# Performance work log

Hardware: AMD Instinct MI355X
Metric: run time of the kernel (lower is better)

The kernel has to match this reference:

```python
import jax, jax.numpy as jnp
import numpy as np

SEQ_LEN = 2048
DIM = 1024
DIM_HEAD = 64
NHEAD = DIM // DIM_HEAD


def setup_inputs() -> dict:
    key = jax.random.key(0)
    k1, k2, k3 = jax.random.split(key, 3)
    x = jax.random.normal(k1, (SEQ_LEN, DIM), dtype=jnp.float32)
    # ortho_init approximated by scaled gaussian weights (same math path in forward)
    Wqkv = jax.random.normal(k2, (DIM, 3 * DIM), dtype=jnp.float32) / np.sqrt(DIM)
    Wout = jax.random.normal(k3, (DIM, DIM), dtype=jnp.float32) / np.sqrt(DIM)
    bias = jnp.zeros((DIM,), dtype=jnp.float32)
    return {"x": x, "Wqkv": Wqkv, "Wout": Wout, "bias": bias}


def reference(x, Wqkv, Wout, bias):
    seq_len = x.shape[-2]
    qkv = x @ Wqkv  # [S, 3*dim]
    qkv = jnp.reshape(qkv, (-1, 3, NHEAD, DIM_HEAD))  # [S,3,H,D]
    qkv = jnp.swapaxes(qkv, 0, 2)  # [H,3,S,D]
    q, k, v = (jax.lax.index_in_dim(qkv, i, -3, keepdims=False) for i in range(3))
    # [H,S,S] full logits, scaled
    logits = q @ jnp.swapaxes(k, -1, -2) / jnp.sqrt(DIM_HEAD)
    mask = jnp.tril(jnp.ones((seq_len, seq_len), dtype=jnp.float32))
    logits = jnp.where(mask, logits, jnp.finfo(logits.dtype).min)
    dtype = logits.dtype
    probs = jax.nn.softmax(logits.astype(jnp.float32), axis=-1).astype(dtype)
    attn_outs = probs @ v  # [H,S,D]
    attn_outs = jnp.reshape(jnp.swapaxes(attn_outs, 0, 1), (-1, NHEAD * DIM_HEAD))
    return attn_outs @ Wout + bias
```

## Files before the change

kernel.cpp:

```cpp
#include <hip/hip_runtime.h>
#include <cstdint>

#define SEQ_LEN 2048
#define DIM 1024
#define NHEAD 16
#define DHEAD 64
#define QKV_LD (3 * DIM)

typedef unsigned short u16;
typedef short bf16x8 __attribute__((ext_vector_type(8)));
typedef float f32x4 __attribute__((ext_vector_type(4)));

__device__ __forceinline__ u16 f2bf(float f) {
    union { float f; unsigned u; } v;
    v.f = f;
    unsigned r = v.u + 0x7fff + ((v.u >> 16) & 1);
    return (u16)(r >> 16);
}

__device__ __forceinline__ void load_lds16(const void* g, void* l) {
    __builtin_amdgcn_global_load_lds(
        (const __attribute__((address_space(1))) void*)g,
        (__attribute__((address_space(3))) void*)l, 16, 0, 0);
}

__global__ __launch_bounds__(256) void cast_bf16_k(const float* __restrict__ in,
                                                   u16* __restrict__ out, int n4) {
    const int i = blockIdx.x * 256 + threadIdx.x;
    if (i < n4) {
        const float4 v = reinterpret_cast<const float4*>(in)[i];
        const unsigned p0 = (unsigned)f2bf(v.x) | ((unsigned)f2bf(v.y) << 16);
        const unsigned p1 = (unsigned)f2bf(v.z) | ((unsigned)f2bf(v.w) << 16);
        reinterpret_cast<uint2*>(out)[i] = make_uint2(p0, p1);
    }
}

__global__ __launch_bounds__(256) void transpose_cast_k(const float* __restrict__ W,
                                                        u16* __restrict__ Wt,
                                                        int K, int N) {
    __shared__ float tile[32][33];
    const int n0 = blockIdx.x * 32, k0 = blockIdx.y * 32;
    const int tx = threadIdx.x & 31, ty = threadIdx.x >> 5;
#pragma unroll
    for (int i = 0; i < 32; i += 8)
        tile[ty + i][tx] = W[(k0 + ty + i) * N + n0 + tx];
    __syncthreads();
#pragma unroll
    for (int i = 0; i < 32; i += 8)
        Wt[(n0 + ty + i) * K + k0 + tx] = f2bf(tile[tx][ty + i]);
}

template <int MODE, int BM, int BN>
__global__ __launch_bounds__(256) void gemm_bf16(const u16* __restrict__ A,
                                                 const u16* __restrict__ Bt,
                                                 const float* __restrict__ bias,
                                                 void* __restrict__ Cout,
                                                 int M, int N, int K) {
    constexpr int AI = BM / 32;
    constexpr int BJ = BN / 32;
    constexpr int ASZ = BM * 64;
    constexpr int BSZ = BN * 64;
    __shared__ u16 As[2 * ASZ];
    __shared__ u16 Bs[2 * BSZ];

    const int t = threadIdx.x;
    const int lane = t & 63;
    const int quad = lane >> 4;
    const int l15 = lane & 15;
    const int w = t >> 6;
    const int wm = (w & 1) * (BM / 2);
    const int wn = (w >> 1) * (BN / 2);
    const int m0 = blockIdx.y * BM;
    const int n0 = blockIdx.x * BN;
    const int sr = t >> 2;
    const int sc = (t & 3) << 3;

    const u16* Ab = A + (size_t)(m0 + sr) * K + sc;
    const u16* Bb = Bt + (size_t)(n0 + sr) * K + sc;

    auto stage = [&](int buf, int k0) {
#pragma unroll
        for (int kc = 0; kc < 2; ++kc) {
#pragma unroll
            for (int c = 0; c < BM / 64; ++c)
                load_lds16(Ab + (size_t)(c * 64) * K + k0 + kc * 32,
                           &As[buf * ASZ + kc * BM * 32 + c * 2048 + t * 8]);
#pragma unroll
            for (int c = 0; c < BN / 64; ++c)
                load_lds16(Bb + (size_t)(c * 64) * K + k0 + kc * 32,
                           &Bs[buf * BSZ + kc * BN * 32 + c * 2048 + t * 8]);
        }
    };

    stage(0, 0);
    f32x4 acc[AI][BJ] = {};

    const int niter = K / 64;
    for (int it = 0; it < niter; ++it) {
        const int cur = it & 1, nxt = cur ^ 1;
        __syncthreads();
        if (it + 1 < niter) stage(nxt, (it + 1) * 64);
#pragma unroll
        for (int kc = 0; kc < 2; ++kc) {
            bf16x8 af[AI], bfr[BJ];
#pragma unroll
            for (int i = 0; i < AI; ++i)
                af[i] = *reinterpret_cast<const bf16x8*>(
                    &As[cur * ASZ + kc * BM * 32 + (wm + i * 16 + l15) * 32 + quad * 8]);
#pragma unroll
            for (int j = 0; j < BJ; ++j)
                bfr[j] = *reinterpret_cast<const bf16x8*>(
                    &Bs[cur * BSZ + kc * BN * 32 + (wn + j * 16 + l15) * 32 + quad * 8]);
#pragma unroll
            for (int i = 0; i < AI; ++i)
#pragma unroll
                for (int j = 0; j < BJ; ++j)
                    acc[i][j] =
                        __builtin_amdgcn_mfma_f32_16x16x32_bf16(af[i], bfr[j], acc[i][j], 0, 0, 0);
        }
    }

#pragma unroll
    for (int j = 0; j < BJ; ++j) {
        const int col = n0 + wn + j * 16 + l15;
        float bv = 0.f;
        if constexpr (MODE == 1) bv = bias[col];
#pragma unroll
        for (int i = 0; i < AI; ++i) {
            const int row = m0 + wm + i * 16 + quad * 4;
#pragma unroll
            for (int r = 0; r < 4; ++r) {
                const float v = acc[i][j][r];
                if constexpr (MODE == 1)
                    ((float*)Cout)[(size_t)(row + r) * N + col] = v + bv;
                else
                    ((u16*)Cout)[(size_t)(row + r) * N + col] = f2bf(v);
            }
        }
    }
}

__global__ __launch_bounds__(256) void attn_mfma(const u16* __restrict__ qkv,
                                                 u16* __restrict__ O) {
    constexpr int PSTR = 40;
    __shared__ u16 SM[2048 + 8192 + 8192 + 4 * 16 * PSTR];
    u16* Qs = SM;
    u16* Ks = SM + 2048;
    u16* Vt = SM + 2048 + 8192;
    u16* Ps = SM + 2048 + 16384;
    float* Ored = (float*)(SM + 2048);
    float* Lred = Ored + 32 * 66;

    const int b = blockIdx.x;
    const int i = 63 - (b >> 4);
    const int h = b & 15;
    const int q0 = i * 32;
    const int jmax = i >> 1;

    const int t = threadIdx.x;
    const int lane = t & 63;
    const int quad = lane >> 4;
    const int l15 = lane & 15;
    const int w = t >> 6;
    const int wq = w >> 1;
    const int wk = w & 1;

    const int sr = t >> 2;
    const int sc = (t & 3) << 3;

    {
        const int qch = t >> 7, qr = (t >> 2) & 31;
        load_lds16(qkv + (size_t)(q0 + qr) * QKV_LD + h * DHEAD + qch * 32 + sc, &Qs[t * 8]);
    }
    const u16* kbase = qkv + (size_t)sr * QKV_LD + DIM + h * DHEAD + sc;
    load_lds16(kbase, &Ks[t * 8]);
    load_lds16(kbase + 32, &Ks[2048 + t * 8]);

    const int vr = lane;
    const int vc = w * 8;
    const u16* vsrc = qkv + (size_t)vr * QKV_LD + 2 * DIM + h * DHEAD + vc;
    uint4 va = *reinterpret_cast<const uint4*>(vsrc);
    uint4 vb = *reinterpret_cast<const uint4*>(vsrc + 32);

    __syncthreads();
    const bf16x8 qf0 = *reinterpret_cast<const bf16x8*>(&Qs[(wq * 16 + l15) * 32 + quad * 8]);
    const bf16x8 qf1 =
        *reinterpret_cast<const bf16x8*>(&Qs[1024 + (wq * 16 + l15) * 32 + quad * 8]);

    {
        const unsigned e[8] = {va.x & 0xffffu, va.x >> 16, va.y & 0xffffu, va.y >> 16,
                               va.z & 0xffffu, va.z >> 16, va.w & 0xffffu, va.w >> 16};
        const unsigned f[8] = {vb.x & 0xffffu, vb.x >> 16, vb.y & 0xffffu, vb.y >> 16,
                               vb.z & 0xffffu, vb.z >> 16, vb.w & 0xffffu, vb.w >> 16};
#pragma unroll
        for (int k = 0; k < 8; ++k) {
            Vt[(vc + k) * 64 + (((vr >> 3) ^ k) << 3) + (vr & 7)] = (u16)e[k];
            Vt[(vc + 32 + k) * 64 + (((vr >> 3) ^ k) << 3) + (vr & 7)] = (u16)f[k];
        }
    }

    f32x4 oacc[4] = {};
    float lsum[4] = {0.f, 0.f, 0.f, 0.f};
    u16* Pw = Ps + w * 16 * PSTR;
    const int rowl_base = (i & 1) * 32 + wq * 16 + quad * 4;
    constexpr float SCL = 0.18033688f;

    for (int jt = 0; jt <= jmax; ++jt) {
        const int cur = jt & 1, nxt = cur ^ 1;
        __syncthreads();

        if (jt < jmax) {
            const int j1 = (jt + 1) * 64;
            const u16* kb = qkv + (size_t)(j1 + sr) * QKV_LD + DIM + h * DHEAD + sc;
            load_lds16(kb, &Ks[nxt * 4096 + t * 8]);
            load_lds16(kb + 32, &Ks[nxt * 4096 + 2048 + t * 8]);
            const u16* vs = qkv + (size_t)(j1 + vr) * QKV_LD + 2 * DIM + h * DHEAD + vc;
            va = *reinterpret_cast<const uint4*>(vs);
            vb = *reinterpret_cast<const uint4*>(vs + 32);
        }

        f32x4 sacc[2] = {};
#pragma unroll
        for (int nn = 0; nn < 2; ++nn) {
            const int krow = (wk * 32 + nn * 16 + l15) * 32 + quad * 8;
            const bf16x8 kf0 = *reinterpret_cast<const bf16x8*>(&Ks[cur * 4096 + krow]);
            sacc[nn] = __builtin_amdgcn_mfma_f32_16x16x32_bf16(qf0, kf0, sacc[nn], 0, 0, 0);
            const bf16x8 kf1 = *reinterpret_cast<const bf16x8*>(&Ks[cur * 4096 + 2048 + krow]);
            sacc[nn] = __builtin_amdgcn_mfma_f32_16x16x32_bf16(qf1, kf1, sacc[nn], 0, 0, 0);
        }

        const bool diag = (jt == jmax);
#pragma unroll
        for (int r = 0; r < 4; ++r) {
            float p0 = sacc[0][r] * SCL, p1 = sacc[1][r] * SCL;
            if (diag) {
                const int rowl = rowl_base + r;
                if (wk * 32 + l15 > rowl) p0 = -1e30f;
                if (wk * 32 + 16 + l15 > rowl) p1 = -1e30f;
            }
            p0 = exp2f(p0);
            p1 = exp2f(p1);
            lsum[r] += p0 + p1;
            Pw[(quad * 4 + r) * PSTR + l15] = f2bf(p0);
            Pw[(quad * 4 + r) * PSTR + 16 + l15] = f2bf(p1);
        }

        if (jt < jmax) {
            const unsigned e[8] = {va.x & 0xffffu, va.x >> 16, va.y & 0xffffu, va.y >> 16,
                                   va.z & 0xffffu, va.z >> 16, va.w & 0xffffu, va.w >> 16};
            const unsigned f[8] = {vb.x & 0xffffu, vb.x >> 16, vb.y & 0xffffu, vb.y >> 16,
                                   vb.z & 0xffffu, vb.z >> 16, vb.w & 0xffffu, vb.w >> 16};
#pragma unroll
            for (int k = 0; k < 8; ++k) {
                Vt[nxt * 4096 + (vc + k) * 64 + (((vr >> 3) ^ k) << 3) + (vr & 7)] = (u16)e[k];
                Vt[nxt * 4096 + (vc + 32 + k) * 64 + (((vr >> 3) ^ k) << 3) + (vr & 7)] =
                    (u16)f[k];
            }
        }

        const bf16x8 pf = *reinterpret_cast<const bf16x8*>(&Pw[l15 * PSTR + quad * 8]);
#pragma unroll
        for (int nd = 0; nd < 4; ++nd) {
            const int dloc = nd * 16 + l15;
            const bf16x8 vf = *reinterpret_cast<const bf16x8*>(
                &Vt[cur * 4096 + dloc * 64 + (((wk * 4 + quad) ^ (dloc & 7)) << 3)]);
            oacc[nd] = __builtin_amdgcn_mfma_f32_16x16x32_bf16(pf, vf, oacc[nd], 0, 0, 0);
        }
    }

#pragma unroll
    for (int r = 0; r < 4; ++r) {
        float l = lsum[r];
#pragma unroll
        for (int off = 1; off < 16; off <<= 1) l += __shfl_xor(l, off, 64);
        lsum[r] = l;
    }
    __syncthreads();
    if (l15 == 0)
#pragma unroll
        for (int r = 0; r < 4; ++r) Lred[wk * 32 + wq * 16 + quad * 4 + r] = lsum[r];
    if (wk == 1)
#pragma unroll
        for (int nd = 0; nd < 4; ++nd)
#pragma unroll
            for (int r = 0; r < 4; ++r)
                Ored[(wq * 16 + quad * 4 + r) * 66 + nd * 16 + l15] = oacc[nd][r];
    __syncthreads();
    if (wk == 0) {
        float inv[4];
#pragma unroll
        for (int r = 0; r < 4; ++r) {
            const int rr = wq * 16 + quad * 4 + r;
            inv[r] = 1.0f / (Lred[rr] + Lred[32 + rr]);
        }
#pragma unroll
        for (int nd = 0; nd < 4; ++nd)
#pragma unroll
            for (int r = 0; r < 4; ++r) {
                const int rr = wq * 16 + quad * 4 + r;
                O[(size_t)(q0 + rr) * DIM + h * DHEAD + nd * 16 + l15] =
                    f2bf((oacc[nd][r] + Ored[rr * 66 + nd * 16 + l15]) * inv[r]);
            }
    }
}

extern "C" void kernel_launch(void* const* d_in, const int* in_sizes, int n_in,
                              void* d_out, int out_size, void* d_ws, size_t ws_size,
                              hipStream_t stream) {
    const float* x = (const float*)d_in[0];
    const float* Wqkv = (const float*)d_in[1];
    const float* Wout = (const float*)d_in[2];
    const float* bias = (const float*)d_in[3];
    float* out = (float*)d_out;

    char* ws = (char*)d_ws;
    u16* xb = (u16*)ws;
    u16* Wqkvt = (u16*)(ws + (4u << 20));
    u16* Woutt = (u16*)(ws + (10u << 20));
    u16* qkvb = (u16*)(ws + (12u << 20));
    u16* Ob = (u16*)(ws + (24u << 20));

    cast_bf16_k<<<(SEQ_LEN * DIM / 4 + 255) / 256, 256, 0, stream>>>(x, xb, SEQ_LEN * DIM / 4);
    transpose_cast_k<<<dim3(QKV_LD / 32, DIM / 32), 256, 0, stream>>>(Wqkv, Wqkvt, DIM, QKV_LD);
    transpose_cast_k<<<dim3(DIM / 32, DIM / 32), 256, 0, stream>>>(Wout, Woutt, DIM, DIM);

    gemm_bf16<0, 128, 64><<<dim3(QKV_LD / 64, SEQ_LEN / 128), 256, 0, stream>>>(
        xb, Wqkvt, nullptr, qkvb, SEQ_LEN, QKV_LD, DIM);

    attn_mfma<<<dim3(64 * NHEAD), 256, 0, stream>>>(qkvb, Ob);

    gemm_bf16<1, 64, 64><<<dim3(DIM / 64, SEQ_LEN / 64), 256, 0, stream>>>(
        Ob, Woutt, bias, out, SEQ_LEN, DIM, DIM);
}
```

Measured before the change: 148.0 us.

## Fuse prep kernels, shrink attention LDS to single buffer, tune QKV GEMM BK

Merges the x cast and both weight transpose-casts into one launch to cut launch overhead. The attention kernel drops its double-buffered K/V shared memory for a single buffer, loading K/V into registers and writing them between barriers. This shrinks LDS so more blocks can be resident. The P tile now uses truncation instead of rounding for bf16, and the QKV GEMM K-tile drops to 32. The single buffer adds two barriers per iteration and truncation slightly changes numerics.

```diff
diff --git a/kernel.cpp b/kernel.cpp
--- a/kernel.cpp
+++ b/kernel.cpp
@@ -24,33 +24,45 @@
         (__attribute__((address_space(3))) void*)l, 16, 0, 0);
 }
 
-__global__ __launch_bounds__(256) void cast_bf16_k(const float* __restrict__ in,
-                                                   u16* __restrict__ out, int n4) {
-    const int i = blockIdx.x * 256 + threadIdx.x;
-    if (i < n4) {
-        const float4 v = reinterpret_cast<const float4*>(in)[i];
+__device__ __forceinline__ void transpose_tile(const float* __restrict__ W,
+                                               u16* __restrict__ Wt, int K, int N,
+                                               int bx, int by, int t, float (*tile)[33]) {
+    const int n0 = bx * 32, k0 = by * 32;
+    const int tx = t & 31, ty = t >> 5;
+#pragma unroll
+    for (int i = 0; i < 32; i += 8)
+        tile[ty + i][tx] = W[(size_t)(k0 + ty + i) * N + n0 + tx];
+    __syncthreads();
+#pragma unroll
+    for (int i = 0; i < 32; i += 8)
+        Wt[(size_t)(n0 + ty + i) * K + k0 + tx] = f2bf(tile[tx][ty + i]);
+}
+
+__global__ __launch_bounds__(256) void prep_k(const float* __restrict__ x,
+                                              const float* __restrict__ Wqkv,
+                                              const float* __restrict__ Wout,
+                                              u16* __restrict__ xb,
+                                              u16* __restrict__ Wqkvt,
+                                              u16* __restrict__ Woutt) {
+    __shared__ float tile[32][33];
+    const int b = blockIdx.x;
+    const int t = threadIdx.x;
+    if (b < 2048) {
+        const int i = b * 256 + t;
+        const float4 v = reinterpret_cast<const float4*>(x)[i];
         const unsigned p0 = (unsigned)f2bf(v.x) | ((unsigned)f2bf(v.y) << 16);
         const unsigned p1 = (unsigned)f2bf(v.z) | ((unsigned)f2bf(v.w) << 16);
-        reinterpret_cast<uint2*>(out)[i] = make_uint2(p0, p1);
-    }
-}
-
-__global__ __launch_bounds__(256) void transpose_cast_k(const float* __restrict__ W,
-                                                        u16* __restrict__ Wt,
-                                                        int K, int N) {
-    __shared__ float tile[32][33];
-    const int n0 = blockIdx.x * 32, k0 = blockIdx.y * 32;
-    const int tx = threadIdx.x & 31, ty = threadIdx.x >> 5;
-#pragma unroll
-    for (int i = 0; i < 32; i += 8)
-        tile[ty + i][tx] = W[(k0 + ty + i) * N + n0 + tx];
-    __syncthreads();
-#pragma unroll
-    for (int i = 0; i < 32; i += 8)
-        Wt[(n0 + ty + i) * K + k0 + tx] = f2bf(tile[tx][ty + i]);
-}
-
-template <int MODE, int BM, int BN>
+        reinterpret_cast<uint2*>(xb)[i] = make_uint2(p0, p1);
+    } else if (b < 5120) {
+        const int b2 = b - 2048;
+        transpose_tile(Wqkv, Wqkvt, DIM, QKV_LD, b2 % 96, b2 / 96, t, tile);
+    } else {
+        const int b3 = b - 5120;
+        transpose_tile(Wout, Woutt, DIM, DIM, b3 & 31, b3 >> 5, t, tile);
+    }
+}
+
+template <int MODE, int BM, int BN, int BK>
 __global__ __launch_bounds__(256) void gemm_bf16(const u16* __restrict__ A,
                                                  const u16* __restrict__ Bt,
                                                  const float* __restrict__ bias,
@@ -58,8 +70,8 @@
                                                  int M, int N, int K) {
     constexpr int AI = BM / 32;
     constexpr int BJ = BN / 32;
-    constexpr int ASZ = BM * 64;
-    constexpr int BSZ = BN * 64;
+    constexpr int ASZ = BM * BK;
+    constexpr int BSZ = BN * BK;
     __shared__ u16 As[2 * ASZ];
     __shared__ u16 Bs[2 * BSZ];
 
@@ -80,7 +92,7 @@
 
     auto stage = [&](int buf, int k0) {
 #pragma unroll
-        for (int kc = 0; kc < 2; ++kc) {
+        for (int kc = 0; kc < BK / 32; ++kc) {
 #pragma unroll
             for (int c = 0; c < BM / 64; ++c)
                 load_lds16(Ab + (size_t)(c * 64) * K + k0 + kc * 32,
@@ -95,13 +107,13 @@
     stage(0, 0);
     f32x4 acc[AI][BJ] = {};
 
-    const int niter = K / 64;
+    const int niter = K / BK;
     for (int it = 0; it < niter; ++it) {
         const int cur = it & 1, nxt = cur ^ 1;
         __syncthreads();
-        if (it + 1 < niter) stage(nxt, (it + 1) * 64);
-#pragma unroll
-        for (int kc = 0; kc < 2; ++kc) {
+        if (it + 1 < niter) stage(nxt, (it + 1) * BK);
+#pragma unroll
+        for (int kc = 0; kc < BK / 32; ++kc) {
             bf16x8 af[AI], bfr[BJ];
 #pragma unroll
             for (int i = 0; i < AI; ++i)
@@ -143,12 +155,11 @@
 __global__ __launch_bounds__(256) void attn_mfma(const u16* __restrict__ qkv,
                                                  u16* __restrict__ O) {
     constexpr int PSTR = 40;
-    __shared__ u16 SM[2048 + 8192 + 8192 + 4 * 16 * PSTR];
-    u16* Qs = SM;
-    u16* Ks = SM + 2048;
-    u16* Vt = SM + 2048 + 8192;
-    u16* Ps = SM + 2048 + 16384;
-    float* Ored = (float*)(SM + 2048);
+    __shared__ u16 SM[2560 + 4096 + 4096];
+    u16* Ps = SM;
+    u16* Ks = SM + 2560;
+    u16* Vt = SM + 2560 + 4096;
+    float* Ored = (float*)SM;
     float* Lred = Ored + 32 * 66;
 
     const int b = blockIdx.x;
@@ -167,37 +178,40 @@
 
     const int sr = t >> 2;
     const int sc = (t & 3) << 3;
-
-    {
-        const int qch = t >> 7, qr = (t >> 2) & 31;
-        load_lds16(qkv + (size_t)(q0 + qr) * QKV_LD + h * DHEAD + qch * 32 + sc, &Qs[t * 8]);
-    }
-    const u16* kbase = qkv + (size_t)sr * QKV_LD + DIM + h * DHEAD + sc;
-    load_lds16(kbase, &Ks[t * 8]);
-    load_lds16(kbase + 32, &Ks[2048 + t * 8]);
-
-    const int vr = lane;
-    const int vc = w * 8;
-    const u16* vsrc = qkv + (size_t)vr * QKV_LD + 2 * DIM + h * DHEAD + vc;
-    uint4 va = *reinterpret_cast<const uint4*>(vsrc);
-    uint4 vb = *reinterpret_cast<const uint4*>(vsrc + 32);
-
-    __syncthreads();
-    const bf16x8 qf0 = *reinterpret_cast<const bf16x8*>(&Qs[(wq * 16 + l15) * 32 + quad * 8]);
+    const int vp = (t & 31) * 2;
+    const int vq = (t >> 5) * 8;
+
+    load_lds16(qkv + (size_t)(q0 + ((t >> 2) & 31)) * QKV_LD + h * DHEAD + (t >> 7) * 32 + sc,
+               &SM[t * 8]);
+    const u16* kp0 = qkv + (size_t)sr * QKV_LD + DIM + h * DHEAD + sc;
+    uint4 ka = *reinterpret_cast<const uint4*>(kp0);
+    uint4 kb = *reinterpret_cast<const uint4*>(kp0 + 32);
+    const u16* vp0 = qkv + (size_t)vp * QKV_LD + 2 * DIM + h * DHEAD + vq;
+    uint4 va = *reinterpret_cast<const uint4*>(vp0);
+    uint4 vb = *reinterpret_cast<const uint4*>(vp0 + QKV_LD);
+
+    __syncthreads();
+    const bf16x8 qf0 = *reinterpret_cast<const bf16x8*>(&SM[(wq * 16 + l15) * 32 + quad * 8]);
     const bf16x8 qf1 =
-        *reinterpret_cast<const bf16x8*>(&Qs[1024 + (wq * 16 + l15) * 32 + quad * 8]);
-
-    {
-        const unsigned e[8] = {va.x & 0xffffu, va.x >> 16, va.y & 0xffffu, va.y >> 16,
-                               va.z & 0xffffu, va.z >> 16, va.w & 0xffffu, va.w >> 16};
-        const unsigned f[8] = {vb.x & 0xffffu, vb.x >> 16, vb.y & 0xffffu, vb.y >> 16,
-                               vb.z & 0xffffu, vb.z >> 16, vb.w & 0xffffu, vb.w >> 16};
-#pragma unroll
-        for (int k = 0; k < 8; ++k) {
-            Vt[(vc + k) * 64 + (((vr >> 3) ^ k) << 3) + (vr & 7)] = (u16)e[k];
-            Vt[(vc + 32 + k) * 64 + (((vr >> 3) ^ k) << 3) + (vr & 7)] = (u16)f[k];
-        }
-    }
+        *reinterpret_cast<const bf16x8*>(&SM[1024 + (wq * 16 + l15) * 32 + quad * 8]);
+    __syncthreads();
+
+    auto writeKV = [&](const uint4& kA, const uint4& kB, const uint4& vA, const uint4& vB) {
+        *reinterpret_cast<uint4*>(&Ks[t * 8]) = kA;
+        *reinterpret_cast<uint4*>(&Ks[2048 + t * 8]) = kB;
+        const unsigned a4[4] = {vA.x, vA.y, vA.z, vA.w};
+        const unsigned b4[4] = {vB.x, vB.y, vB.z, vB.w};
+#pragma unroll
+        for (int idx = 0; idx < 8; ++idx) {
+            const unsigned lo = (idx & 1) ? (a4[idx >> 1] >> 16) : (a4[idx >> 1] & 0xffffu);
+            const unsigned hi = (idx & 1) ? (b4[idx >> 1] >> 16) : (b4[idx >> 1] & 0xffffu);
+            const int d = vq + idx;
+            const int pos = d * 64 + (((vp >> 3) ^ (d & 7)) << 3) + (vp & 7);
+            *reinterpret_cast<unsigned*>(&Vt[pos]) = lo | (hi << 16);
+        }
+    };
+    writeKV(ka, kb, va, vb);
+    __syncthreads();
 
     f32x4 oacc[4] = {};
     float lsum[4] = {0.f, 0.f, 0.f, 0.f};
@@ -206,26 +220,23 @@
     constexpr float SCL = 0.18033688f;
 
     for (int jt = 0; jt <= jmax; ++jt) {
-        const int cur = jt & 1, nxt = cur ^ 1;
-        __syncthreads();
-
         if (jt < jmax) {
             const int j1 = (jt + 1) * 64;
-            const u16* kb = qkv + (size_t)(j1 + sr) * QKV_LD + DIM + h * DHEAD + sc;
-            load_lds16(kb, &Ks[nxt * 4096 + t * 8]);
-            load_lds16(kb + 32, &Ks[nxt * 4096 + 2048 + t * 8]);
-            const u16* vs = qkv + (size_t)(j1 + vr) * QKV_LD + 2 * DIM + h * DHEAD + vc;
-            va = *reinterpret_cast<const uint4*>(vs);
-            vb = *reinterpret_cast<const uint4*>(vs + 32);
+            const u16* kp = qkv + (size_t)(j1 + sr) * QKV_LD + DIM + h * DHEAD + sc;
+            ka = *reinterpret_cast<const uint4*>(kp);
+            kb = *reinterpret_cast<const uint4*>(kp + 32);
+            const u16* vpt = qkv + (size_t)(j1 + vp) * QKV_LD + 2 * DIM + h * DHEAD + vq;
+            va = *reinterpret_cast<const uint4*>(vpt);
+            vb = *reinterpret_cast<const uint4*>(vpt + QKV_LD);
         }
 
         f32x4 sacc[2] = {};
 #pragma unroll
         for (int nn = 0; nn < 2; ++nn) {
             const int krow = (wk * 32 + nn * 16 + l15) * 32 + quad * 8;
-            const bf16x8 kf0 = *reinterpret_cast<const bf16x8*>(&Ks[cur * 4096 + krow]);
+            const bf16x8 kf0 = *reinterpret_cast<const bf16x8*>(&Ks[krow]);
             sacc[nn] = __builtin_amdgcn_mfma_f32_16x16x32_bf16(qf0, kf0, sacc[nn], 0, 0, 0);
-            const bf16x8 kf1 = *reinterpret_cast<const bf16x8*>(&Ks[cur * 4096 + 2048 + krow]);
+            const bf16x8 kf1 = *reinterpret_cast<const bf16x8*>(&Ks[2048 + krow]);
             sacc[nn] = __builtin_amdgcn_mfma_f32_16x16x32_bf16(qf1, kf1, sacc[nn], 0, 0, 0);
         }
 
@@ -241,21 +252,8 @@
             p0 = exp2f(p0);
             p1 = exp2f(p1);
             lsum[r] += p0 + p1;
-            Pw[(quad * 4 + r) * PSTR + l15] = f2bf(p0);
-            Pw[(quad * 4 + r) * PSTR + 16 + l15] = f2bf(p1);
-        }
-
-        if (jt < jmax) {
-            const unsigned e[8] = {va.x & 0xffffu, va.x >> 16, va.y & 0xffffu, va.y >> 16,
-                                   va.z & 0xffffu, va.z >> 16, va.w & 0xffffu, va.w >> 16};
-            const unsigned f[8] = {vb.x & 0xffffu, vb.x >> 16, vb.y & 0xffffu, vb.y >> 16,
-                                   vb.z & 0xffffu, vb.z >> 16, vb.w & 0xffffu, vb.w >> 16};
-#pragma unroll
-            for (int k = 0; k < 8; ++k) {
-                Vt[nxt * 4096 + (vc + k) * 64 + (((vr >> 3) ^ k) << 3) + (vr & 7)] = (u16)e[k];
-                Vt[nxt * 4096 + (vc + 32 + k) * 64 + (((vr >> 3) ^ k) << 3) + (vr & 7)] =
-                    (u16)f[k];
-            }
+            Pw[(quad * 4 + r) * PSTR + l15] = (u16)(__float_as_uint(p0) >> 16);
+            Pw[(quad * 4 + r) * PSTR + 16 + l15] = (u16)(__float_as_uint(p1) >> 16);
         }
 
         const bf16x8 pf = *reinterpret_cast<const bf16x8*>(&Pw[l15 * PSTR + quad * 8]);
@@ -263,8 +261,14 @@
         for (int nd = 0; nd < 4; ++nd) {
             const int dloc = nd * 16 + l15;
             const bf16x8 vf = *reinterpret_cast<const bf16x8*>(
-                &Vt[cur * 4096 + dloc * 64 + (((wk * 4 + quad) ^ (dloc & 7)) << 3)]);
+                &Vt[dloc * 64 + (((wk * 4 + quad) ^ (dloc & 7)) << 3)]);
             oacc[nd] = __builtin_amdgcn_mfma_f32_16x16x32_bf16(pf, vf, oacc[nd], 0, 0, 0);
+        }
+
+        if (jt < jmax) {
+            __syncthreads();
+            writeKV(ka, kb, va, vb);
+            __syncthreads();
         }
     }
 
@@ -320,15 +324,13 @@
     u16* qkvb = (u16*)(ws + (12u << 20));
     u16* Ob = (u16*)(ws + (24u << 20));
 
-    cast_bf16_k<<<(SEQ_LEN * DIM / 4 + 255) / 256, 256, 0, stream>>>(x, xb, SEQ_LEN * DIM / 4);
-    transpose_cast_k<<<dim3(QKV_LD / 32, DIM / 32), 256, 0, stream>>>(Wqkv, Wqkvt, DIM, QKV_LD);
-    transpose_cast_k<<<dim3(DIM / 32, DIM / 32), 256, 0, stream>>>(Wout, Woutt, DIM, DIM);
-
-    gemm_bf16<0, 128, 64><<<dim3(QKV_LD / 64, SEQ_LEN / 128), 256, 0, stream>>>(
+    prep_k<<<dim3(6144), 256, 0, stream>>>(x, Wqkv, Wout, xb, Wqkvt, Woutt);
+
+    gemm_bf16<0, 128, 64, 32><<<dim3(QKV_LD / 64, SEQ_LEN / 128), 256, 0, stream>>>(
         xb, Wqkvt, nullptr, qkvb, SEQ_LEN, QKV_LD, DIM);
 
     attn_mfma<<<dim3(64 * NHEAD), 256, 0, stream>>>(qkvb, Ob);
 
-    gemm_bf16<1, 64, 64><<<dim3(DIM / 64, SEQ_LEN / 64), 256, 0, stream>>>(
+    gemm_bf16<1, 64, 64, 64><<<dim3(DIM / 64, SEQ_LEN / 64), 256, 0, stream>>>(
         Ob, Woutt, bias, out, SEQ_LEN, DIM, DIM);
 }
```

Measured after the change: 151.6 us. +2.4%, slower.
